# Optimization experiments

Measured on AMD Instinct MI355X. Metric: run time of the kernel, lower is better.

Reference implementation:

```python
import jax, jax.numpy as jnp
import numpy as np

B, S, HID, H, D, KC = 2, 4096, 2048, 16, 128, 4
EPS = 1e-5


def causal_dw_conv(x, kern):
    # x: (b, s, C); kern: (K, 1, C) depthwise causal conv
    K = kern.shape[0]
    xp = jnp.pad(x, ((0, 0), (K - 1, 0), (0, 0)))
    return jax.lax.conv_general_dilated(
        xp, kern, (1,), 'VALID',
        dimension_numbers=('NWC', 'WIO', 'NWC'),
        feature_group_count=x.shape[-1])


def l2norm(x):
    return x * jax.lax.rsqrt(jnp.sum(x * x, -1, keepdims=True) + 1e-6)


def chunk_delta(q, k, v, g, beta, chunk_size):
    # q,k,v,g: (b,s,h,d); beta: (b,s,h). Chunked gated delta-rule (WY repr).
    dt0 = q.dtype
    q = jnp.transpose(q, (0, 2, 1, 3)).astype(jnp.float32)
    k = jnp.transpose(k, (0, 2, 1, 3)).astype(jnp.float32)
    v = jnp.transpose(v, (0, 2, 1, 3)).astype(jnp.float32)
    g = jnp.transpose(g, (0, 2, 1, 3)).astype(jnp.float32)
    beta = jnp.transpose(beta, (0, 2, 1)).astype(jnp.float32)
    b, h, s, dk = k.shape
    dv = v.shape[-1]
    C = chunk_size
    pad = (C - s % C) % C
    if pad:
        p4 = ((0, 0), (0, 0), (0, pad), (0, 0))
        q = jnp.pad(q, p4); k = jnp.pad(k, p4)
        v = jnp.pad(v, p4); g = jnp.pad(g, p4)
        beta = jnp.pad(beta, ((0, 0), (0, 0), (0, pad)))
    n = (s + pad) // C
    q = q * dk ** -0.5

    def toc(x):  # (b,h,s,d) -> (n,b,h,C,d)
        return jnp.transpose(x.reshape(b, h, n, C, -1), (2, 0, 1, 3, 4))

    g_cum = jnp.cumsum(g.reshape(b, h, n, C, dk), axis=-2)  # per-chunk cumsum
    xs = (toc(q), toc(k), toc(v),
          jnp.transpose(g_cum, (2, 0, 1, 3, 4)),
          jnp.transpose(beta.reshape(b, h, n, C), (2, 0, 1, 3)))
    eye = jnp.eye(C, dtype=jnp.float32)
    strict = jnp.tril(jnp.ones((C, C), bool), -1)[:, :, None]  # i > j
    incl = jnp.tril(jnp.ones((C, C), bool))[:, :, None]        # i >= j
    neg_inf = -jnp.inf

    def body(Sst, xc):
        qc, kc, vc, g_i, bc = xc  # (b,h,C,dk/dv), bc (b,h,C)
        gd = g_i[..., :, None, :] - g_i[..., None, :, :]       # (b,h,C,C,dk)
        A = jnp.einsum('bhijd,bhid,bhjd->bhij',
                       jnp.exp(jnp.where(strict, gd, neg_inf)), kc, kc)
        A = A * bc[..., None]
        L = eye + A  # unit lower-triangular
        T = jax.scipy.linalg.solve_triangular(
            L, jnp.broadcast_to(eye, L.shape), lower=True)
        Tf = T * bc[..., None, :]
        u = Tf @ vc                           # (b,h,C,dv)
        w = Tf @ (kc * jnp.exp(g_i))          # (b,h,C,dk)
        v_new = u - w @ Sst                   # (b,h,C,dv)
        attn = jnp.einsum('bhijd,bhid,bhjd->bhij',
                          jnp.exp(jnp.where(incl, gd, neg_inf)), qc, kc)
        o = attn @ v_new + (qc * jnp.exp(g_i)) @ Sst
        g_last = g_i[..., -1:, :]             # (b,h,1,dk)
        k_tail = kc * jnp.exp(g_last - g_i)
        S_new = Sst * jnp.exp(g_last[..., 0, :])[..., None] \
              + jnp.einsum('bhcd,bhce->bhde', k_tail, v_new)
        return S_new, o

    S0 = jnp.zeros((b, h, dk, dv), jnp.float32)
    _, o = jax.lax.scan(jax.checkpoint(body), S0, xs)
    o = jnp.transpose(o, (1, 2, 0, 3, 4)).reshape(b, h, -1, dv)[:, :, :s]
    return jnp.transpose(o, (0, 2, 1, 3)).astype(dt0)


def _forward(hidden_states, Wq, Wk, Wv, conv_q, conv_k, conv_v, Wb,
             Wfa, Wfb, Wga, Wgb, bgb, A_log, dt_bias, rms_scale, Wo,
             chunk_size):
    x = hidden_states
    b, s, _ = x.shape
    q = jax.nn.silu(causal_dw_conv(x @ Wq, conv_q)).reshape(b, s, H, D)
    k = jax.nn.silu(causal_dw_conv(x @ Wk, conv_k)).reshape(b, s, H, D)
    v = jax.nn.silu(causal_dw_conv(x @ Wv, conv_v)).reshape(b, s, H, D)
    q, k = l2norm(q), l2norm(k)
    beta = jax.nn.sigmoid(x @ Wb)                     # (b,s,H)
    g_lin = (x @ Wfa) @ Wfb + dt_bias                 # fused KDA gate (log space)
    g = -jnp.exp(A_log) * jax.nn.softplus(
        g_lin.astype(jnp.float32)).reshape(b, s, H, D)
    core = chunk_delta(q, k, v, g, beta, chunk_size)  # (b,s,H,D)
    gate = ((x @ Wga) @ Wgb + bgb).reshape(b, s, H, D)
    cf = core.astype(jnp.float32)
    normed = cf * jax.lax.rsqrt(
        jnp.mean(cf * cf, -1, keepdims=True) + EPS) * rms_scale
    o = normed * jax.nn.sigmoid(gate.astype(jnp.float32))
    return o.reshape(b, s, H * D) @ Wo


def setup_inputs() -> dict:
    key = jax.random.key(0)
    ks = jax.random.split(key, 18)
    def w(k, shape, fan_in):
        return jax.random.normal(k, shape, jnp.float32) * fan_in ** -0.5
    return {
        'hidden_states': jax.random.normal(ks[0], (B, S, HID), jnp.float32),
        'Wq': w(ks[1], (HID, H * D), HID),
        'Wk': w(ks[2], (HID, H * D), HID),
        'Wv': w(ks[3], (HID, H * D), HID),
        'conv_q': w(ks[4], (KC, 1, H * D), KC),
        'conv_k': w(ks[5], (KC, 1, H * D), KC),
        'conv_v': w(ks[6], (KC, 1, H * D), KC),
        'Wb': w(ks[7], (HID, H), HID),
        'Wfa': w(ks[8], (HID, D), HID),
        'Wfb': w(ks[9], (D, H * D), D),
        'Wga': w(ks[10], (HID, D), HID),
        'Wgb': w(ks[11], (D, H * D), D),
        'bgb': jnp.zeros((H * D,), jnp.float32),
        'A_log': jnp.log(jax.random.uniform(ks[12], (1, 1, H, 1),
                                            jnp.float32, 0.5, 8.0)),
        'dt_bias': jnp.ones((H * D,), jnp.float32),
        'rms_scale': jnp.ones((D,), jnp.float32),
        'Wo': w(ks[13], (H * D, HID), H * D),
        'chunk_size': 64,
    }


def reference(hidden_states, Wq, Wk, Wv, conv_q, conv_k, conv_v, Wb,
              Wfa, Wfb, Wga, Wgb, bgb, A_log, dt_bias, rms_scale, Wo,
              chunk_size):
    return _forward(hidden_states, Wq, Wk, Wv, conv_q, conv_k, conv_v, Wb,
                    Wfa, Wfb, Wga, Wgb, bgb, A_log, dt_bias, rms_scale, Wo,
                    int(chunk_size))
```

## Files before the change

kernel.cpp:

```cpp
#include <hip/hip_runtime.h>
#include <hip/hip_bf16.h>

typedef __hip_bfloat16 bf16;
typedef __attribute__((ext_vector_type(4))) float f32x4;
typedef __attribute__((ext_vector_type(8))) short short8;

#define TOT   8192
#define SEQ   4096
#define NHD   16
#define HD    128
#define C2    2048
#define CHK   64
#define NCPB  64
#define SW    16
#define QSCALE 0.08838834764831845f

__device__ __forceinline__ float b2f(bf16 x){ return __bfloat162float(x); }
__device__ __forceinline__ bf16  f2b(float x){ return __float2bfloat16(x); }
__device__ __forceinline__ float expn(float x){ return __expf(fminf(x, 0.f)); }
__device__ __forceinline__ short bts(float x){
  bf16 b = f2b(x); short s; __builtin_memcpy(&s, &b, 2); return s;
}
__device__ __forceinline__ float s2f(short v){
  unsigned int u = ((unsigned int)(unsigned short)v) << 16;
  float f; __builtin_memcpy(&f, &u, 4); return f;
}

__device__ __attribute__((aligned(16))) unsigned short G_xb  [TOT*C2];
__device__ __attribute__((aligned(16))) unsigned short G_xlo [TOT*C2];
__device__ __attribute__((aligned(16))) unsigned short G_qlin[TOT*C2];
__device__ __attribute__((aligned(16))) unsigned short G_klin[TOT*C2];
__device__ __attribute__((aligned(16))) unsigned short G_vlin[TOT*C2];
__device__ __attribute__((aligned(16))) unsigned short G_qb  [TOT*C2];
__device__ __attribute__((aligned(16))) unsigned short G_kb  [TOT*C2];
__device__ __attribute__((aligned(16))) unsigned short G_vb  [TOT*C2];
__device__ __attribute__((aligned(16))) unsigned short G_qg  [TOT*C2];
__device__ __attribute__((aligned(16))) unsigned short G_gate[TOT*C2];
__device__ __attribute__((aligned(16))) unsigned short G_core[TOT*C2];
__device__ __attribute__((aligned(16))) unsigned short G_opre[TOT*C2];
__device__ __attribute__((aligned(16))) float          G_g   [TOT*C2];
__device__ __attribute__((aligned(16))) unsigned short G_attn[2048*CHK*CHK];
__device__ __attribute__((aligned(16))) unsigned short G_ktt [2048*CHK*HD];
__device__ __attribute__((aligned(16))) float          G_egl [2048*HD];
__device__ __attribute__((aligned(16))) float          G_beta[TOT*NHD];
__device__ __attribute__((aligned(16))) unsigned short G_fah [TOT*HD];
__device__ __attribute__((aligned(16))) unsigned short G_fal [TOT*HD];
__device__ __attribute__((aligned(16))) unsigned short G_ga  [TOT*HD];
__device__ __attribute__((aligned(16))) unsigned short G_Wqt [C2*C2];
__device__ __attribute__((aligned(16))) unsigned short G_Wkt [C2*C2];
__device__ __attribute__((aligned(16))) unsigned short G_Wvt [C2*C2];
__device__ __attribute__((aligned(16))) unsigned short G_Wot [C2*C2];
__device__ __attribute__((aligned(16))) unsigned short G_Wgat  [HD*C2];
__device__ __attribute__((aligned(16))) unsigned short G_Wbt   [16*C2];
__device__ __attribute__((aligned(16))) unsigned short G_Wfat_h[HD*C2];
__device__ __attribute__((aligned(16))) unsigned short G_Wfat_l[HD*C2];
__device__ __attribute__((aligned(16))) unsigned short G_Wfbt_h[C2*HD];
__device__ __attribute__((aligned(16))) unsigned short G_Wfbt_l[C2*HD];
__device__ __attribute__((aligned(16))) unsigned short G_Wgbt  [C2*HD];

#define P_QLIN ((bf16*)G_qlin)
#define P_KLIN ((bf16*)G_klin)
#define P_VLIN ((bf16*)G_vlin)
#define P_QB   ((bf16*)G_qb)
#define P_KB   ((bf16*)G_kb)
#define P_VB   ((bf16*)G_vb)
#define P_QG   ((bf16*)G_qg)
#define P_GATE ((bf16*)G_gate)
#define P_CORE ((bf16*)G_core)
#define P_OPRE ((bf16*)G_opre)
#define P_ATTN ((bf16*)G_attn)
#define P_KTT  ((bf16*)G_ktt)
#define P_FAH  ((bf16*)G_fah)
#define P_FAL  ((bf16*)G_fal)
#define P_GA   ((bf16*)G_ga)

__device__ __forceinline__ const bf16* selWt(int s){
  switch(s){ case 0: return (const bf16*)G_Wqt; case 1: return (const bf16*)G_Wkt;
             case 2: return (const bf16*)G_Wvt; }
  return (const bf16*)G_Wot;
}
__device__ __forceinline__ bf16* selCm(int s){
  switch(s){ case 0: return P_QLIN; case 1: return P_KLIN; }
  return P_VLIN;
}
__device__ __forceinline__ bf16* selWT(int s){
  switch(s){
    case 0: return (bf16*)G_Wqt;     case 1: return (bf16*)G_Wkt;
    case 2: return (bf16*)G_Wvt;     case 3: return (bf16*)G_Wot;
    case 4: return (bf16*)G_Wgat;    case 5: return (bf16*)G_Wbt;
    case 6: return (bf16*)G_Wfat_h;  case 7: return (bf16*)G_Wfat_l;
    case 8: return (bf16*)G_Wfbt_h;  case 9: return (bf16*)G_Wfbt_l;
  }
  return (bf16*)G_Wgbt;
}

__global__ void __launch_bounds__(256) wtrans_k(const float* __restrict__ W,
                                                int selH, int selL, int N, int K)
{
  __shared__ float tile[64][65];
  const int t = threadIdx.x;
  const int n0 = blockIdx.x*64, k0 = blockIdx.y*64;
  const int c4 = (t&15)*4, rr = t>>4;
  if (n0 + c4 < N){
    #pragma unroll
    for (int i=0;i<4;i++){
      const float* src = W + (size_t)(k0+rr+16*i)*N + n0 + c4;
      float4 f = *(const float4*)src;
      tile[rr+16*i][c4+0]=f.x; tile[rr+16*i][c4+1]=f.y;
      tile[rr+16*i][c4+2]=f.z; tile[rr+16*i][c4+3]=f.w;
    }
  }
  __syncthreads();
  bf16* outH = selWT(selH);
  bf16* outL = (selL >= 0) ? selWT(selL) : nullptr;
  const int nr = t>>3, kc = (t&7)*8;
  #pragma unroll
  for (int p=0;p<2;p++){
    int n = p*32 + nr;
    if (n0 + n < N){
      __attribute__((aligned(16))) bf16 tmpH[8];
      __attribute__((aligned(16))) bf16 tmpL[8];
      #pragma unroll
      for (int j=0;j<8;j++){
        float v = tile[kc+j][n];
        bf16 hh = f2b(v);
        tmpH[j] = hh;
        tmpL[j] = f2b(v - b2f(hh));
      }
      *(float4*)(outH + (size_t)(n0+n)*K + k0 + kc) = *(const float4*)tmpH;
      if (outL)
        *(float4*)(outL + (size_t)(n0+n)*K + k0 + kc) = *(const float4*)tmpL;
    }
  }
}

__global__ void __launch_bounds__(256) xconv_k(const float* __restrict__ x)
{
  size_t idx = ((size_t)blockIdx.x*256 + threadIdx.x)*8;
  const float* src = x + idx;
  float4 f0 = *(const float4*)src, f1 = *(const float4*)(src+4);
  float v[8] = {f0.x,f0.y,f0.z,f0.w,f1.x,f1.y,f1.z,f1.w};
  __attribute__((aligned(16))) bf16 th[8];
  __attribute__((aligned(16))) bf16 tl[8];
  #pragma unroll
  for (int u=0;u<8;u++){
    bf16 h = f2b(v[u]);
    th[u] = h;
    tl[u] = f2b(v[u] - b2f(h));
  }
  *(float4*)((bf16*)G_xb  + idx) = *(const float4*)th;
  *(float4*)((bf16*)G_xlo + idx) = *(const float4*)tl;
}

template<int OUTMODE>
__global__ void __launch_bounds__(256) gemm_mfma(
    int aSel, int bSel, int cSel, float* __restrict__ Cw, int N)
{
  const bf16* A  = (aSel==0) ? (const bf16*)G_xb : (const bf16*)G_opre;
  const bf16* Bt = selWt(bSel);
  __shared__ bf16 As[128*40];
  __shared__ bf16 Bs[128*40];
  const int t  = threadIdx.x;
  const int l  = t & 63;
  const int wv = t >> 6;
  const int wm = (wv>>1)*64, wn = (wv&1)*64;
  const int bm = blockIdx.y*128, bn = blockIdx.x*128;
  const int lr = l & 15;
  const int lk = (l>>4)*8;
  const int sr = t>>1, sc = (t&1)*16;

  f32x4 acc[4][4];
  #pragma unroll
  for (int i=0;i<4;i++)
    #pragma unroll
    for (int j=0;j<4;j++)
      #pragma unroll
      for (int v=0;v<4;v++) acc[i][j][v] = 0.f;

  for (int k0=0; k0<C2; k0+=32){
    const bf16* ga = A  + (size_t)(bm+sr)*C2 + k0 + sc;
    const bf16* gb = Bt + (size_t)(bn+sr)*C2 + k0 + sc;
    float4 a0 = *(const float4*)ga; float4 a1 = *(const float4*)(ga+8);
    float4 b0 = *(const float4*)gb; float4 b1 = *(const float4*)(gb+8);
    __syncthreads();
    *(float4*)&As[sr*40+sc]   = a0; *(float4*)&As[sr*40+sc+8] = a1;
    *(float4*)&Bs[sr*40+sc]   = b0; *(float4*)&Bs[sr*40+sc+8] = b1;
    __syncthreads();
    short8 af[4], bfr[4];
    #pragma unroll
    for (int i=0;i<4;i++){
      af[i]  = *(const short8*)&As[(wm+i*16+lr)*40 + lk];
      bfr[i] = *(const short8*)&Bs[(wn+i*16+lr)*40 + lk];
    }
    #pragma unroll
    for (int i=0;i<4;i++)
      #pragma unroll
      for (int j=0;j<4;j++)
        acc[i][j] = __builtin_amdgcn_mfma_f32_16x16x32_bf16(af[i], bfr[j], acc[i][j], 0, 0, 0);
  }

  bf16* Cb = (OUTMODE==0) ? selCm(cSel) : nullptr;
  #pragma unroll
  for (int i=0;i<4;i++){
    #pragma unroll
    for (int v=0;v<4;v++){
      int r = bm + wm + i*16 + (l>>4)*4 + v;
      #pragma unroll
      for (int j=0;j<4;j++){
        int col = bn + wn + j*16 + (l&15);
        float val = acc[i][j][v];
        if (OUTMODE==1) Cw[(size_t)r*N + col] = val;
        else            Cb[(size_t)r*N + col] = f2b(val);
      }
    }
  }
}

__global__ void __launch_bounds__(256) thinx_k()
{
  const int t = threadIdx.x;
  const int l = t & 63;
  const int wv = t >> 6;
  const int rb = wv >> 1, nh = wv & 1;
  const int lane16 = l & 15, quad = l >> 4;
  const int bm = blockIdx.x*32;
  const int arow = bm + rb*16 + lane16;

  const bf16* Ah = (const bf16*)G_xb  + (size_t)arow*C2;
  const bf16* Al = (const bf16*)G_xlo + (size_t)arow*C2;
  const bf16* Wfh = (const bf16*)G_Wfat_h;
  const bf16* Wfl = (const bf16*)G_Wfat_l;
  const bf16* Wg  = (const bf16*)G_Wgat;
  const bf16* Wbp = (const bf16*)G_Wbt;

  f32x4 accF[4], accG[4], accB;
  #pragma unroll
  for (int cb=0;cb<4;cb++)
    #pragma unroll
    for (int v=0;v<4;v++){ accF[cb][v]=0.f; accG[cb][v]=0.f; }
  #pragma unroll
  for (int v=0;v<4;v++) accB[v]=0.f;

  for (int k0=0; k0<C2; k0+=32){
    const int ko = k0 + quad*8;
    short8 ah = *(const short8*)(Ah + ko);
    short8 al = *(const short8*)(Al + ko);
    #pragma unroll
    for (int cb=0;cb<4;cb++){
      const size_t nrow = (size_t)(nh*64 + cb*16 + lane16)*C2 + ko;
      short8 bh = *(const short8*)(Wfh + nrow);
      short8 bl = *(const short8*)(Wfl + nrow);
      accF[cb] = __builtin_amdgcn_mfma_f32_16x16x32_bf16(ah, bh, accF[cb], 0,0,0);
      accF[cb] = __builtin_amdgcn_mfma_f32_16x16x32_bf16(ah, bl, accF[cb], 0,0,0);
      accF[cb] = __builtin_amdgcn_mfma_f32_16x16x32_bf16(al, bh, accF[cb], 0,0,0);
      short8 bg = *(const short8*)(Wg + nrow);
      accG[cb] = __builtin_amdgcn_mfma_f32_16x16x32_bf16(ah, bg, accG[cb], 0,0,0);
    }
    if (nh == 0){
      short8 bb = *(const short8*)(Wbp + (size_t)lane16*C2 + ko);
      accB = __builtin_amdgcn_mfma_f32_16x16x32_bf16(ah, bb, accB, 0,0,0);
    }
  }

  #pragma unroll
  for (int cb=0;cb<4;cb++){
    #pragma unroll
    for (int v=0;v<4;v++){
      int r = bm + rb*16 + quad*4 + v;
      int n = nh*64 + cb*16 + lane16;
      float vf = accF[cb][v];
      bf16 fh = f2b(vf);
      P_FAH[(size_t)r*HD + n] = fh;
      P_FAL[(size_t)r*HD + n] = f2b(vf - b2f(fh));
      P_GA [(size_t)r*HD + n] = f2b(accG[cb][v]);
    }
  }
  if (nh == 0){
    #pragma unroll
    for (int v=0;v<4;v++){
      int r = bm + rb*16 + quad*4 + v;
      G_beta[(size_t)r*NHD + lane16] = 1.f/(1.f + __expf(-accB[v]));
    }
  }
}

__global__ void __launch_bounds__(256) glin_k(const float* __restrict__ dtb)
{
  const int t = threadIdx.x;
  const int l = t & 63;
  const int wv = t >> 6;
  const int wm = (wv>>1)*64, wn = (wv&1)*64;
  const int bm = blockIdx.y*128, bn = blockIdx.x*128;
  const int lane16 = l & 15, quad = l >> 4;

  f32x4 acc[4][4];
  #pragma unroll
  for (int i=0;i<4;i++)
    #pragma unroll
    for (int j=0;j<4;j++)
      #pragma unroll
      for (int v=0;v<4;v++) acc[i][j][v]=0.f;

  #pragma unroll
  for (int pass=0; pass<3; ++pass){
    const bf16* A = (pass < 2) ? P_FAH : P_FAL;
    const bf16* B = (pass == 1) ? (const bf16*)G_Wfbt_l : (const bf16*)G_Wfbt_h;
    #pragma unroll
    for (int ks=0; ks<4; ++ks){
      short8 af[4], bfr[4];
      #pragma unroll
      for (int i=0;i<4;i++)
        af[i] = *(const short8*)(A + (size_t)(bm+wm+i*16+lane16)*HD + ks*32 + quad*8);
      #pragma unroll
      for (int j=0;j<4;j++)
        bfr[j] = *(const short8*)(B + (size_t)(bn+wn+j*16+lane16)*HD + ks*32 + quad*8);
      #pragma unroll
      for (int i=0;i<4;i++)
        #pragma unroll
        for (int j=0;j<4;j++)
          acc[i][j] = __builtin_amdgcn_mfma_f32_16x16x32_bf16(af[i], bfr[j], acc[i][j], 0,0,0);
    }
  }

  #pragma unroll
  for (int i=0;i<4;i++){
    #pragma unroll
    for (int v=0;v<4;v++){
      int r = bm + wm + i*16 + quad*4 + v;
      #pragma unroll
      for (int j=0;j<4;j++){
        int n = bn + wn + j*16 + lane16;
        G_g[(size_t)r*C2 + n] = acc[i][j][v] + dtb[n];
      }
    }
  }
}

__global__ void __launch_bounds__(256) gate_k(const float* __restrict__ bgb)
{
  const int t = threadIdx.x;
  const int l = t & 63;
  const int wv = t >> 6;
  const int wm = (wv>>1)*64, wn = (wv&1)*64;
  const int bm = blockIdx.y*128, bn = blockIdx.x*128;
  const int lane16 = l & 15, quad = l >> 4;

  f32x4 acc[4][4];
  #pragma unroll
  for (int i=0;i<4;i++)
    #pragma unroll
    for (int j=0;j<4;j++)
      #pragma unroll
      for (int v=0;v<4;v++) acc[i][j][v]=0.f;

  const bf16* A = P_GA;
  const bf16* B = (const bf16*)G_Wgbt;
  #pragma unroll
  for (int ks=0; ks<4; ++ks){
    short8 af[4], bfr[4];
    #pragma unroll
    for (int i=0;i<4;i++)
      af[i] = *(const short8*)(A + (size_t)(bm+wm+i*16+lane16)*HD + ks*32 + quad*8);
    #pragma unroll
    for (int j=0;j<4;j++)
      bfr[j] = *(const short8*)(B + (size_t)(bn+wn+j*16+lane16)*HD + ks*32 + quad*8);
    #pragma unroll
    for (int i=0;i<4;i++)
      #pragma unroll
      for (int j=0;j<4;j++)
        acc[i][j] = __builtin_amdgcn_mfma_f32_16x16x32_bf16(af[i], bfr[j], acc[i][j], 0,0,0);
  }

  #pragma unroll
  for (int i=0;i<4;i++){
    #pragma unroll
    for (int v=0;v<4;v++){
      int r = bm + wm + i*16 + quad*4 + v;
      #pragma unroll
      for (int j=0;j<4;j++){
        int n = bn + wn + j*16 + lane16;
        P_GATE[(size_t)r*C2 + n] = f2b(acc[i][j][v] + bgb[n]);
      }
    }
  }
}

__global__ void __launch_bounds__(256) conv_silu_k(
    int sel, const float* __restrict__ kern, int do_norm)
{
  const bf16* lin = sel==0 ? P_QLIN : sel==1 ? P_KLIN : P_VLIN;
  bf16*       out = sel==0 ? P_QB   : sel==1 ? P_KB   : P_VB;

  __shared__ float part[256];
  __shared__ float scal[16];
  const int t = threadIdx.x;
  const int r = blockIdx.x;
  const int s = r & (SEQ-1);
  const int c0 = t*8;
  float v[8];
  #pragma unroll
  for (int u=0;u<8;u++) v[u]=0.f;
  for (int j=0;j<4;j++){
    int sp = s - 3 + j;
    if (sp < 0) continue;
    const bf16* row = lin + (size_t)(r-3+j)*C2 + c0;
    const float* kr = kern + j*C2 + c0;
    #pragma unroll
    for (int u=0;u<8;u++) v[u] += b2f(row[u]) * kr[u];
  }
  #pragma unroll
  for (int u=0;u<8;u++){ float x=v[u]; v[u] = x / (1.f + __expf(-x)); }
  if (do_norm) {
    float ss=0.f;
    #pragma unroll
    for (int u=0;u<8;u++) ss += v[u]*v[u];
    part[t]=ss; __syncthreads();
    if (t<16){
      float s2=0.f;
      for (int i=0;i<16;i++) s2 += part[t*16+i];
      scal[t] = rsqrtf(s2 + 1e-6f);
    }
    __syncthreads();
    float sc = scal[t>>4];
    #pragma unroll
    for (int u=0;u<8;u++) v[u] *= sc;
  }
  bf16* orow = out + (size_t)r*C2 + c0;
  #pragma unroll
  for (int u=0;u<8;u++) orow[u] = f2b(v[u]);
}

__global__ void __launch_bounds__(256) g_transform_k(const float* __restrict__ A_log)
{
  size_t i = (size_t)blockIdx.x*256 + threadIdx.x;
  float x = fminf(G_g[i], 80.f);
  int h = (int)((i >> 7) & (NHD-1));
  float a = __expf(A_log[h]);
  float sp = (x > 20.f) ? x : log1pf(__expf(x));
  G_g[i] = -a * sp;
}

__global__ void __launch_bounds__(128) gcum_k()
{
  const int blk = blockIdx.x;
  const int icg = blk & 127, h = blk >> 7;
  const int d = threadIdx.x;
  size_t gi = (size_t)(icg*CHK)*C2 + h*HD + d;
  float a = 0.f;
  for (int r=0;r<CHK;r++){ a += G_g[gi]; G_g[gi] = a; gi += C2; }
}

__global__ void __launch_bounds__(512, 4) stage1_k()
{
  __shared__ __attribute__((aligned(16))) char sm[63872];
  bf16*  kT   = (bf16*)sm;
  bf16*  qT   = (bf16*)(sm+17408);
  float* AmD  = (float*)(sm+17408);
  float* AmL  = (float*)(sm+21760);
  float* gH   = (float*)(sm+34816);
  float* Dinv = (float*)(sm+34816);
  bf16*  cJ   = (bf16*)(sm+44544);
  float* rhs  = (float*)(sm+44544);
  float* rS   = (float*)(sm+57600);
  float* er   = (float*)(sm+61440);
  float* bcs  = (float*)(sm+63552);

  const int blk = blockIdx.x;
  const int h   = blk >> 7;
  const int icg = blk & 127;
  const int cid = blk;
  const int t   = threadIdx.x;
  const int l   = t & 63;
  const int wv  = t >> 6;
  const int lane16 = l & 15, quad = l >> 4;
  const size_t base = (size_t)(icg*CHK)*C2 + h*HD;

  const int ci_b = t >> 7;
  const int ck   = t & 127;
  int ci, cjj;
  {
    float fi = (sqrtf(8.f*(float)ck + 1.f) - 1.f)*0.5f;
    ci = (int)fi;
    cjj = ck - ((ci*(ci+1))>>1);
    if (cjj < 0){ ci--; cjj = ck - ((ci*(ci+1))>>1); }
    if (cjj > ci){ ci++; cjj = ck - ((ci*(ci+1))>>1); }
  }
  const int hasB = (ck < 8);
  const int bjB  = 8 + ck;

  #pragma unroll
  for (int it=0; it<2; ++it){
    int e = t + 512*it;
    int r = e >> 4, c8 = (e & 15)*8;
    *(float4*)&kT[r*136 + c8] = *(const float4*)(P_KB + base + (size_t)r*C2 + c8);
    *(float4*)&qT[r*136 + c8] = *(const float4*)(P_QB + base + (size_t)r*C2 + c8);
  }
  if (t < 64) bcs[t] = G_beta[(size_t)(icg*CHK + t)*NHD + h];

  float aaA=0.f, qqA=0.f, aaB=0.f, qqB=0.f;

  #pragma unroll 1
  for (int p=0; p<4; ++p){
    const int dq0 = p*32;
    __syncthreads();
    { int r = t >> 3, f4 = (t & 7)*4;
      float4 f = *(const float4*)(G_g + base + (size_t)r*C2 + dq0 + f4);
      gH[r*38 + f4+0] = f.x; gH[r*38 + f4+1] = f.y;
      gH[r*38 + f4+2] = f.z; gH[r*38 + f4+3] = f.w;
    }
    __syncthreads();
    if (t < 128){
      int I = t >> 5, dd = t & 31;
      float rv = gH[(I*16)*38 + dd];
      rS[I*132 + dq0 + dd] = rv;
      er[I*132 + dq0 + dd] = expn(rv);
    }
    if (t < 32) G_egl[(size_t)cid*HD + dq0 + t] = expn(gH[63*38 + t]);
    {
      const int rI = 16*ci_b + ci, rJ = 16*ci_b + cjj;
      const float* gRi = &gH[rI*38];
      const float* gRj = &gH[rJ*38];
      const bf16*  kRi = &kT[rI*136 + dq0];
      const bf16*  kRj = &kT[rJ*136 + dq0];
      const bf16*  qRi = &qT[rI*136 + dq0];
      float aa = aaA, qq = qqA;
      #pragma unroll 4
      for (int dd=0; dd<32; ++dd){
        float e  = expn(gRi[dd] - gRj[dd]);
        float tk = e * b2f(kRj[dd]);
        aa += tk * b2f(kRi[dd]);
        qq += tk * b2f(qRi[dd]);
      }
      aaA = aa; qqA = qq;
      if (hasB){
        const int rB = 16*ci_b + 15, rJ2 = 16*ci_b + bjB;
        const float* gRi2 = &gH[rB*38];
        const float* gRj2 = &gH[rJ2*38];
        const bf16*  kRi2 = &kT[rB*136 + dq0];
        const bf16*  kRj2 = &kT[rJ2*136 + dq0];
        const bf16*  qRi2 = &qT[rB*136 + dq0];
        float aa2 = aaB, qq2 = qqB;
        #pragma unroll 4
        for (int dd=0; dd<32; ++dd){
          float e  = expn(gRi2[dd] - gRj2[dd]);
          float tk = e * b2f(kRj2[dd]);
          aa2 += tk * b2f(kRi2[dd]);
          qq2 += tk * b2f(qRi2[dd]);
        }
        aaB = aa2; qqB = qq2;
      }
    }
    #pragma unroll
    for (int it=0; it<3; ++it){
      int e = t + 512*it;
      int r = e >> 5, dd = e & 31;
      float rv = gH[(((r>>4)+1)*16)*38 + dd];
      float v = b2f(kT[r*136 + dq0 + dd]) * expn(rv - gH[r*38 + dd]);
      cJ[r*136 + dq0 + dd] = f2b(v);
    }
    {
      int d = t >> 4, r4 = (t & 15)*4;
      float gl = gH[63*38 + d];
      __attribute__((aligned(8))) bf16 tmp[4];
      #pragma unroll
      for (int u=0; u<4; ++u){
        int r = r4 + u;
        tmp[u] = f2b(b2f(kT[r*136 + dq0 + d]) * expn(gl - gH[r*38 + d]));
      }
      *(float2*)(P_KTT + (size_t)cid*(CHK*HD) + (size_t)(dq0 + d)*64 + r4) =
          *(const float2*)tmp;
    }
    __syncthreads();
    #pragma unroll
    for (int it=0; it<4; ++it){
      int e = t + 512*it;
      int r = e >> 5, dd = e & 31;
      int I = r >> 4;
      float eD  = expn(gH[r*38 + dd] - gH[(I*16)*38 + dd]);
      float erv = er[I*132 + dq0 + dd];
      int idx = r*136 + dq0 + dd;
      float av = b2f(kT[idx]) * eD;
      kT[idx] = f2b(av);
      float qv = QSCALE * b2f(qT[idx]) * eD;
      qT[idx] = f2b(qv);
      P_QG[base + (size_t)r*C2 + dq0 + dd] = f2b(qv * erv);
    }
  }
  __syncthreads();

  short8 bfr[4];
  int pI = 0, pJ = 0;
  {
    const int PI_[6] = {1,2,2,3,3,3};
    const int PJ_[6] = {0,0,1,0,1,2};
    if (wv < 6){
      pI = PI_[wv]; pJ = PJ_[wv];
      #pragma unroll
      for (int ks=0; ks<4; ++ks){
        int k0 = ks*32 + quad*8;
        short8 raw = *(const short8*)&cJ[(16*pJ + lane16)*136 + k0];
        short8 o;
        #pragma unroll
        for (int u=0; u<8; ++u){
          int d = k0 + u;
          float m = expn(rS[pI*132 + d] - rS[(pJ+1)*132 + d]);
          o[u] = bts(s2f(raw[u]) * m);
        }
        bfr[ks] = o;
      }
      f32x4 acc;
      #pragma unroll
      for (int v=0; v<4; ++v) acc[v] = 0.f;
      #pragma unroll
      for (int ks=0; ks<4; ++ks){
        short8 af = *(const short8*)&qT[(16*pI + lane16)*136 + ks*32 + quad*8];
        acc = __builtin_amdgcn_mfma_f32_16x16x32_bf16(af, bfr[ks], acc, 0,0,0);
      }
      #pragma unroll
      for (int v=0; v<4; ++v){
        int row = 16*pI + quad*4 + v, col = 16*pJ + lane16;
        P_ATTN[(size_t)cid*4096 + row*64 + col] = f2b(acc[v]);
      }
    } else {
      const int UI_[6] = {0,0,0,1,1,2};
      const int UJ_[6] = {1,2,3,2,3,3};
      float4 zf; zf.x = zf.y = zf.z = zf.w = 0.f;
      int tt = t - 384;
      for (int e = tt; e < 192; e += 128){
        int b = e >> 5, row = (e>>1)&15, hf = e&1;
        *(float4*)(P_ATTN + (size_t)cid*4096 +
                   (size_t)((16*UI_[b]+row)*64 + 16*UJ_[b] + hf*8)) = zf;
      }
    }
    size_t ab = (size_t)cid*4096;
    int rA = 16*ci_b + ci, cA = 16*ci_b + cjj;
    P_ATTN[ab + rA*64 + cA] = f2b(qqA * QSCALE);
    if (ci != cjj) P_ATTN[ab + cA*64 + rA] = f2b(0.f);
    if (hasB){
      int rB = 16*ci_b + 15, cB = 16*ci_b + bjB;
      P_ATTN[ab + rB*64 + cB] = f2b(qqB * QSCALE);
      if (bjB != 15) P_ATTN[ab + cB*64 + rB] = f2b(0.f);
    }
  }
  __syncthreads();

  if (wv < 6){
    f32x4 acc;
    #pragma unroll
    for (int v=0; v<4; ++v) acc[v] = 0.f;
    #pragma unroll
    for (int ks=0; ks<4; ++ks){
      short8 af = *(const short8*)&kT[(16*pI + lane16)*136 + ks*32 + quad*8];
      acc = __builtin_amdgcn_mfma_f32_16x16x32_bf16(af, bfr[ks], acc, 0,0,0);
    }
    #pragma unroll
    for (int v=0; v<4; ++v){
      int r16 = quad*4 + v;
      AmL[wv*272 + r16*17 + lane16] = acc[v] * bcs[16*pI + r16];
    }
  }
  if (ci != cjj) AmD[ci_b*272 + ci*17 + cjj] = aaA * bcs[16*ci_b + ci];
  if (hasB && bjB != 15) AmD[ci_b*272 + 15*17 + bjB] = aaB * bcs[16*ci_b + 15];
  __syncthreads();

  if (wv == 0){
    const int b = l >> 4, col = l & 15;
    const float* Ab = &AmD[b*272];
    float x[16];
    #pragma unroll
    for (int i=0; i<16; ++i){
      float a = (i == col) ? 1.f : 0.f;
      #pragma unroll
      for (int kk=0; kk<i; ++kk)
        a -= Ab[i*17 + kk] * x[kk];
      x[i] = a;
      Dinv[b*272 + i*17 + col] = a;
    }
  }

  #pragma unroll 1
  for (int inst=0; inst<4; ++inst){
    const int isW = inst >> 1;
    const int c0  = (inst & 1) * 64;
    __syncthreads();
    {
      const int r = t >> 3, c8 = (t & 7)*8;
      const float bcv = bcs[r];
      if (!isW){
        float4 f = *(const float4*)(P_VB + base + (size_t)r*C2 + c0 + c8);
        const bf16* e8 = (const bf16*)&f;
        #pragma unroll
        for (int u=0; u<8; ++u) rhs[r*66 + c8 + u] = b2f(e8[u]) * bcv;
      } else {
        const int I = r >> 4;
        #pragma unroll
        for (int u=0; u<8; ++u){
          int d = c0 + c8 + u;
          rhs[r*66 + c8 + u] = b2f(kT[r*136 + d]) * er[I*132 + d] * bcv;
        }
      }
    }
    __syncthreads();
    #pragma unroll 1
    for (int I=0; I<4; ++I){
      if (I > 0){
        #pragma unroll
        for (int e2=0; e2<2; ++e2){
          int slot = t + 512*e2;
          int r16 = slot >> 6, c = slot & 63;
          float a = rhs[(16*I + r16)*66 + c];
          #pragma unroll 1
          for (int J=0; J<I; ++J){
            const float* Arow = &AmL[(J + ((I*(I-1))>>1))*272 + r16*17];
            #pragma unroll
            for (int kk=0; kk<16; ++kk)
              a -= Arow[kk] * rhs[(16*J + kk)*66 + c];
          }
          rhs[(16*I + r16)*66 + c] = a;
        }
        __syncthreads();
      }
      float accv[2];
      #pragma unroll
      for (int e2=0; e2<2; ++e2){
        int slot = t + 512*e2;
        int r16 = slot >> 6, c = slot & 63;
        const float* Drow = &Dinv[I*272 + r16*17];
        float a = 0.f;
        #pragma unroll
        for (int kk=0; kk<16; ++kk)
          a += Drow[kk] * rhs[(16*I + kk)*66 + c];
        accv[e2] = a;
      }
      __syncthreads();
      #pragma unroll
      for (int e2=0; e2<2; ++e2){
        int slot = t + 512*e2;
        rhs[(16*I + (slot>>6))*66 + (slot & 63)] = accv[e2];
      }
      __syncthreads();
    }
    {
      const int r = t >> 3, c8 = (t & 7)*8;
      __attribute__((aligned(16))) bf16 tmp[8];
      #pragma unroll
      for (int u=0; u<8; ++u) tmp[u] = f2b(rhs[r*66 + c8 + u]);
      bf16* dst = isW ? P_QB : P_VB;
      *(float4*)(dst + base + (size_t)r*C2 + c0 + c8) = *(const float4*)tmp;
    }
  }
}

__global__ void __launch_bounds__(256) stage2_k()
{
  __shared__ float Sf[SW][HD+4];
  __shared__ bf16  wqL[CHK][HD+8];
  __shared__ bf16  ktL[HD][CHK+8];
  __shared__ bf16  ashL[CHK][CHK+8];
  __shared__ bf16  vnT[SW][CHK+8];
  __shared__ bf16  uL[CHK][SW+4];
  __shared__ float egl[HD];

  const int blk = blockIdx.x;
  const int batch = blk >> 7;
  const int h  = (blk >> 3) & 15;
  const int sl = blk & 7;
  const int c0 = sl*SW;
  const int t  = threadIdx.x;
  const int l  = t & 63;
  const int wv = t >> 6;
  const int lane16 = l & 15, quad = l >> 4;
  const int R = wv*16;

  for (int i=t;i<SW*(HD+4);i+=256) ((float*)Sf)[i] = 0.f;

  for (int ic=0; ic<NCPB; ic++){
    const int icg = batch*NCPB + ic;
    const int cid = h*128 + icg;
    const size_t rbase = (size_t)(icg*CHK)*C2 + h*HD;

    float4 qgr[4];
    #pragma unroll
    for (int it=0; it<4; ++it){
      int e = (t + 256*it)*8;
      int r = e >> 7, d = e & 127;
      *(float4*)&wqL[r][d] = *(const float4*)(P_QB + rbase + (size_t)r*C2 + d);
      qgr[it] = *(const float4*)(P_QG + rbase + (size_t)r*C2 + d);
    }
    {
      const bf16* src = P_KTT + (size_t)cid*(CHK*HD);
      #pragma unroll
      for (int it=0; it<4; ++it){
        int e = (t + 256*it)*8;
        int d = e >> 6, r = e & 63;
        *(float4*)&ktL[d][r] = *(const float4*)(src + e);
      }
      const bf16* asrc = P_ATTN + (size_t)cid*(CHK*CHK);
      #pragma unroll
      for (int it=0; it<2; ++it){
        int e = (t + 256*it)*8;
        int i2 = e >> 6, j2 = e & 63;
        *(float4*)&ashL[i2][j2] = *(const float4*)(asrc + e);
      }
      int r = t>>2, c = (t&3)*4;
      const bf16* us = P_VB + rbase + (size_t)r*C2 + c0 + c;
      uL[r][c]=us[0]; uL[r][c+1]=us[1]; uL[r][c+2]=us[2]; uL[r][c+3]=us[3];
      if (t < HD) egl[t] = G_egl[(size_t)cid*HD + t];
    }
    __syncthreads();

    {
      f32x4 acc1;
      #pragma unroll
      for (int v=0;v<4;v++) acc1[v]=0.f;
      #pragma unroll
      for (int ks=0; ks<4; ++ks){
        const int k0 = ks*32;
        short8 af = *(const short8*)&wqL[R+lane16][k0 + quad*8];
        short8 bfr;
        #pragma unroll
        for (int j2=0;j2<8;j2++) bfr[j2] = bts(Sf[lane16][k0 + quad*8 + j2]);
        acc1 = __builtin_amdgcn_mfma_f32_16x16x32_bf16(af, bfr, acc1, 0,0,0);
      }
      #pragma unroll
      for (int v=0;v<4;v++){
        int j = R + quad*4 + v;
        float x = b2f(uL[j][lane16]) - acc1[v];
        vnT[lane16][j] = f2b(x);
      }
    }
    __syncthreads();

    #pragma unroll
    for (int it=0; it<4; ++it){
      int e = (t + 256*it)*8;
      int r = e >> 7, d = e & 127;
      *(float4*)&wqL[r][d] = qgr[it];
    }
    __syncthreads();

    {
      f32x4 acc2;
      #pragma unroll
      for (int v=0;v<4;v++) acc2[v]=0.f;
      #pragma unroll
      for (int ks=0; ks<2; ++ks){
        const int k0 = ks*32;
        short8 af = *(const short8*)&ashL[R+lane16][k0 + quad*8];
        short8 bfr = *(const short8*)&vnT[lane16][k0 + quad*8];
        acc2 = __builtin_amdgcn_mfma_f32_16x16x32_bf16(af, bfr, acc2, 0,0,0);
      }
      #pragma unroll
      for (int ks=0; ks<4; ++ks){
        const int k0 = ks*32;
        short8 af = *(const short8*)&wqL[R+lane16][k0 + quad*8];
        short8 bfr;
        #pragma unroll
        for (int j2=0;j2<8;j2++) bfr[j2] = bts(Sf[lane16][k0 + quad*8 + j2]);
        acc2 = __builtin_amdgcn_mfma_f32_16x16x32_bf16(af, bfr, acc2, 0,0,0);
      }
      #pragma unroll
      for (int v=0;v<4;v++){
        size_t row = (size_t)(icg*CHK) + R + quad*4 + v;
        P_CORE[row*C2 + h*HD + c0 + lane16] = f2b(acc2[v]);
      }
    }
    {
      f32x4 accS[2];
      #pragma unroll
      for (int p=0;p<2;p++)
        #pragma unroll
        for (int v=0;v<4;v++) accS[p][v]=0.f;
      #pragma unroll
      for (int p=0;p<2;p++){
        const int dt = wv*2 + p;
        #pragma unroll
        for (int ks=0; ks<2; ++ks){
          const int k0 = ks*32;
          short8 af = *(const short8*)&ktL[dt*16 + lane16][k0 + quad*8];
          short8 bfr = *(const short8*)&vnT[lane16][k0 + quad*8];
          accS[p] = __builtin_amdgcn_mfma_f32_16x16x32_bf16(af, bfr, accS[p], 0,0,0);
        }
      }
      __syncthreads();
      #pragma unroll
      for (int p=0;p<2;p++){
        #pragma unroll
        for (int v=0;v<4;v++){
          int d = (wv*2+p)*16 + quad*4 + v;
          Sf[lane16][d] = Sf[lane16][d]*egl[d] + accS[p][v];
        }
      }
    }
  }
}

__global__ void __launch_bounds__(256) rms_gate_k(const float* __restrict__ rms)
{
  __shared__ float part[256];
  __shared__ float scal[16];
  const int t = threadIdx.x;
  const size_t tok = blockIdx.x;
  const int c0 = t*8;
  float v[8];
  const bf16* cr = P_CORE + tok*C2 + c0;
  #pragma unroll
  for (int u=0;u<8;u++) v[u] = b2f(cr[u]);
  float ss=0.f;
  #pragma unroll
  for (int u=0;u<8;u++) ss += v[u]*v[u];
  part[t]=ss; __syncthreads();
  if (t<16){
    float s2=0.f;
    for (int i=0;i<16;i++) s2 += part[t*16+i];
    scal[t] = rsqrtf(s2*(1.f/HD) + 1e-5f);
  }
  __syncthreads();
  float sc = scal[t>>4];
  const bf16* gr = P_GATE + tok*C2 + c0;
  bf16* orow = P_OPRE + tok*C2 + c0;
  #pragma unroll
  for (int u=0;u<8;u++){
    int d = (c0+u)&127;
    float gv = b2f(gr[u]);
    float x = v[u]*sc*rms[d];
    x *= 1.f/(1.f+__expf(-gv));
    orow[u] = f2b(x);
  }
}

extern "C" void kernel_launch(void* const* d_in, const int* in_sizes, int n_in,
                              void* d_out, int out_size, void* d_ws, size_t ws_size,
                              hipStream_t stream)
{
  const float* x     = (const float*)d_in[0];
  const float* Wq    = (const float*)d_in[1];
  const float* Wk    = (const float*)d_in[2];
  const float* Wv    = (const float*)d_in[3];
  const float* convq = (const float*)d_in[4];
  const float* convk = (const float*)d_in[5];
  const float* convv = (const float*)d_in[6];
  const float* Wb    = (const float*)d_in[7];
  const float* Wfa   = (const float*)d_in[8];
  const float* Wfb   = (const float*)d_in[9];
  const float* Wga   = (const float*)d_in[10];
  const float* Wgb   = (const float*)d_in[11];
  const float* bgb   = (const float*)d_in[12];
  const float* A_log = (const float*)d_in[13];
  const float* dtb   = (const float*)d_in[14];
  const float* rms   = (const float*)d_in[15];
  const float* Wo    = (const float*)d_in[16];
  (void)d_ws; (void)ws_size;

  dim3 gM(16, TOT/128);
  dim3 gN(16, TOT/128);

  wtrans_k<<<dim3(32,32), 256, 0, stream>>>(Wq,  0, -1, C2,  C2);
  wtrans_k<<<dim3(32,32), 256, 0, stream>>>(Wk,  1, -1, C2,  C2);
  wtrans_k<<<dim3(32,32), 256, 0, stream>>>(Wv,  2, -1, C2,  C2);
  wtrans_k<<<dim3(32,32), 256, 0, stream>>>(Wo,  3, -1, C2,  C2);
  wtrans_k<<<dim3(2,32),  256, 0, stream>>>(Wga, 4, -1, HD,  C2);
  wtrans_k<<<dim3(1,32),  256, 0, stream>>>(Wb,  5, -1, NHD, C2);
  wtrans_k<<<dim3(2,32),  256, 0, stream>>>(Wfa, 6,  7, HD,  C2);
  wtrans_k<<<dim3(32,2),  256, 0, stream>>>(Wfb, 8,  9, C2,  HD);
  wtrans_k<<<dim3(32,2),  256, 0, stream>>>(Wgb, 10,-1, C2,  HD);

  xconv_k<<<TOT*C2/(256*8), 256, 0, stream>>>(x);

  gemm_mfma<0><<<gM, 256, 0, stream>>>(0, 0, 0, nullptr, C2);
  gemm_mfma<0><<<gM, 256, 0, stream>>>(0, 1, 1, nullptr, C2);
  gemm_mfma<0><<<gM, 256, 0, stream>>>(0, 2, 2, nullptr, C2);

  thinx_k<<<TOT/32, 256, 0, stream>>>();

  conv_silu_k<<<TOT, 256, 0, stream>>>(0, convq, 1);
  conv_silu_k<<<TOT, 256, 0, stream>>>(1, convk, 1);
  conv_silu_k<<<TOT, 256, 0, stream>>>(2, convv, 0);

  glin_k<<<gN, 256, 0, stream>>>(dtb);
  g_transform_k<<<(TOT*C2)/256, 256, 0, stream>>>(A_log);
  gcum_k<<<2048, 128, 0, stream>>>();

  stage1_k<<<2048, 512, 0, stream>>>();
  stage2_k<<<256, 256, 0, stream>>>();

  gate_k<<<gN, 256, 0, stream>>>(bgb);
  rms_gate_k<<<TOT, 256, 0, stream>>>(rms);

  gemm_mfma<1><<<gM, 256, 0, stream>>>(1, 3, -1, (float*)d_out, C2);
}
```

Measured before the change: 1.575 ms.

## Use direct-to-LDS loads in GEMM, fuse g transform, restructure stage1 diagonal

The main GEMM now loads A and B tiles with global_load_lds straight into unpadded LDS and swizzles block order into groups of eight for cache locality. The separate g_transform kernel is folded into the glin_k epilogue, which saves a full fp32 read and write pass over the g tensor. In stage1, the diagonal-block intra-chunk dot products are remapped so each thread handles a pair of adjacent columns with vectorized loads. Removing the LDS padding may add bank conflicts on the fragment reads, and the GEMM still uses a single LDS buffer with no double buffering.

```diff
diff --git a/kernel.cpp b/kernel.cpp
--- a/kernel.cpp
+++ b/kernel.cpp
@@ -24,6 +24,12 @@
 __device__ __forceinline__ float s2f(short v){
   unsigned int u = ((unsigned int)(unsigned short)v) << 16;
   float f; __builtin_memcpy(&f, &u, 4); return f;
+}
+__device__ __forceinline__ void gload_lds16(const void* g, void* l){
+  __builtin_amdgcn_global_load_lds(
+    (const __attribute__((address_space(1))) unsigned int*)g,
+    (__attribute__((address_space(3))) unsigned int*)l,
+    16, 0, 0);
 }
 
 __device__ __attribute__((aligned(16))) unsigned short G_xb  [TOT*C2];
@@ -158,16 +164,23 @@
 {
   const bf16* A  = (aSel==0) ? (const bf16*)G_xb : (const bf16*)G_opre;
   const bf16* Bt = selWt(bSel);
-  __shared__ bf16 As[128*40];
-  __shared__ bf16 Bs[128*40];
+  __shared__ bf16 As[128*32];
+  __shared__ bf16 Bs[128*32];
   const int t  = threadIdx.x;
   const int l  = t & 63;
   const int wv = t >> 6;
   const int wm = (wv>>1)*64, wn = (wv&1)*64;
-  const int bm = blockIdx.y*128, bn = blockIdx.x*128;
+
+  const int nbx = gridDim.x;
+  const int tot = nbx * gridDim.y;
+  const int id  = blockIdx.y*nbx + blockIdx.x;
+  const int cpx = tot >> 3;
+  const int sw  = (id & 7)*cpx + (id >> 3);
+  const int bm  = (sw / nbx)*128, bn = (sw % nbx)*128;
+
   const int lr = l & 15;
   const int lk = (l>>4)*8;
-  const int sr = t>>1, sc = (t&1)*16;
+  const int srow = l >> 2, scol = (l & 3)*8;
 
   f32x4 acc[4][4];
   #pragma unroll
@@ -178,19 +191,19 @@
       for (int v=0;v<4;v++) acc[i][j][v] = 0.f;
 
   for (int k0=0; k0<C2; k0+=32){
-    const bf16* ga = A  + (size_t)(bm+sr)*C2 + k0 + sc;
-    const bf16* gb = Bt + (size_t)(bn+sr)*C2 + k0 + sc;
-    float4 a0 = *(const float4*)ga; float4 a1 = *(const float4*)(ga+8);
-    float4 b0 = *(const float4*)gb; float4 b1 = *(const float4*)(gb+8);
     __syncthreads();
-    *(float4*)&As[sr*40+sc]   = a0; *(float4*)&As[sr*40+sc+8] = a1;
-    *(float4*)&Bs[sr*40+sc]   = b0; *(float4*)&Bs[sr*40+sc+8] = b1;
+    #pragma unroll
+    for (int i=0;i<2;i++){
+      const int rb = wv*32 + i*16;
+      gload_lds16(A  + (size_t)(bm + rb + srow)*C2 + k0 + scol, &As[rb*32]);
+      gload_lds16(Bt + (size_t)(bn + rb + srow)*C2 + k0 + scol, &Bs[rb*32]);
+    }
     __syncthreads();
     short8 af[4], bfr[4];
     #pragma unroll
     for (int i=0;i<4;i++){
-      af[i]  = *(const short8*)&As[(wm+i*16+lr)*40 + lk];
-      bfr[i] = *(const short8*)&Bs[(wn+i*16+lr)*40 + lk];
+      af[i]  = *(const short8*)&As[(wm+i*16+lr)*32 + lk];
+      bfr[i] = *(const short8*)&Bs[(wn+i*16+lr)*32 + lk];
     }
     #pragma unroll
     for (int i=0;i<4;i++)
@@ -284,7 +297,8 @@
   }
 }
 
-__global__ void __launch_bounds__(256) glin_k(const float* __restrict__ dtb)
+__global__ void __launch_bounds__(256) glin_k(const float* __restrict__ dtb,
+                                              const float* __restrict__ A_log)
 {
   const int t = threadIdx.x;
   const int l = t & 63;
@@ -323,14 +337,18 @@
   }
 
   #pragma unroll
-  for (int i=0;i<4;i++){
-    #pragma unroll
-    for (int v=0;v<4;v++){
-      int r = bm + wm + i*16 + quad*4 + v;
-      #pragma unroll
-      for (int j=0;j<4;j++){
-        int n = bn + wn + j*16 + lane16;
-        G_g[(size_t)r*C2 + n] = acc[i][j][v] + dtb[n];
+  for (int j=0;j<4;j++){
+    const int n = bn + wn + j*16 + lane16;
+    const float dtv = dtb[n];
+    const float av = __expf(A_log[(n>>7)&(NHD-1)]);
+    #pragma unroll
+    for (int i=0;i<4;i++){
+      #pragma unroll
+      for (int v=0;v<4;v++){
+        int r = bm + wm + i*16 + quad*4 + v;
+        float x = fminf(acc[i][j][v] + dtv, 80.f);
+        float sp = (x > 20.f) ? x : log1pf(__expf(x));
+        G_g[(size_t)r*C2 + n] = -av * sp;
       }
     }
   }
@@ -428,16 +446,6 @@
   bf16* orow = out + (size_t)r*C2 + c0;
   #pragma unroll
   for (int u=0;u<8;u++) orow[u] = f2b(v[u]);
-}
-
-__global__ void __launch_bounds__(256) g_transform_k(const float* __restrict__ A_log)
-{
-  size_t i = (size_t)blockIdx.x*256 + threadIdx.x;
-  float x = fminf(G_g[i], 80.f);
-  int h = (int)((i >> 7) & (NHD-1));
-  float a = __expf(A_log[h]);
-  float sp = (x > 20.f) ? x : log1pf(__expf(x));
-  G_g[i] = -a * sp;
 }
 
 __global__ void __launch_bounds__(128) gcum_k()
@@ -475,18 +483,20 @@
   const int lane16 = l & 15, quad = l >> 4;
   const size_t base = (size_t)(icg*CHK)*C2 + h*HD;
 
-  const int ci_b = t >> 7;
-  const int ck   = t & 127;
-  int ci, cjj;
-  {
-    float fi = (sqrtf(8.f*(float)ck + 1.f) - 1.f)*0.5f;
-    ci = (int)fi;
-    cjj = ck - ((ci*(ci+1))>>1);
-    if (cjj < 0){ ci--; cjj = ck - ((ci*(ci+1))>>1); }
-    if (cjj > ci){ ci++; cjj = ck - ((ci*(ci+1))>>1); }
-  }
-  const int hasB = (ck < 8);
-  const int bjB  = 8 + ck;
+  const bool dvalid = (t < 288);
+  int dbq = 0, di = 0, dj0 = 0;
+  bool dhas1 = false;
+  if (dvalid){
+    dbq = t / 72;
+    int s = t - dbq*72;
+    #pragma unroll
+    for (int m=0;m<16;m++){
+      int np = (m+2)>>1;
+      if (s >= np){ s -= np; di = m+1; }
+    }
+    dj0 = 2*s;
+    dhas1 = (dj0 + 1 <= di);
+  }
 
   #pragma unroll
   for (int it=0; it<2; ++it){
@@ -497,7 +507,7 @@
   }
   if (t < 64) bcs[t] = G_beta[(size_t)(icg*CHK + t)*NHD + h];
 
-  float aaA=0.f, qqA=0.f, aaB=0.f, qqB=0.f;
+  float aa0=0.f, qq0=0.f, aa1=0.f, qq1=0.f;
 
   #pragma unroll 1
   for (int p=0; p<4; ++p){
@@ -516,38 +526,34 @@
       er[I*132 + dq0 + dd] = expn(rv);
     }
     if (t < 32) G_egl[(size_t)cid*HD + dq0 + t] = expn(gH[63*38 + t]);
-    {
-      const int rI = 16*ci_b + ci, rJ = 16*ci_b + cjj;
-      const float* gRi = &gH[rI*38];
-      const float* gRj = &gH[rJ*38];
-      const bf16*  kRi = &kT[rI*136 + dq0];
-      const bf16*  kRj = &kT[rJ*136 + dq0];
-      const bf16*  qRi = &qT[rI*136 + dq0];
-      float aa = aaA, qq = qqA;
-      #pragma unroll 4
-      for (int dd=0; dd<32; ++dd){
-        float e  = expn(gRi[dd] - gRj[dd]);
-        float tk = e * b2f(kRj[dd]);
-        aa += tk * b2f(kRi[dd]);
-        qq += tk * b2f(qRi[dd]);
-      }
-      aaA = aa; qqA = qq;
-      if (hasB){
-        const int rB = 16*ci_b + 15, rJ2 = 16*ci_b + bjB;
-        const float* gRi2 = &gH[rB*38];
-        const float* gRj2 = &gH[rJ2*38];
-        const bf16*  kRi2 = &kT[rB*136 + dq0];
-        const bf16*  kRj2 = &kT[rJ2*136 + dq0];
-        const bf16*  qRi2 = &qT[rB*136 + dq0];
-        float aa2 = aaB, qq2 = qqB;
-        #pragma unroll 4
-        for (int dd=0; dd<32; ++dd){
-          float e  = expn(gRi2[dd] - gRj2[dd]);
-          float tk = e * b2f(kRj2[dd]);
-          aa2 += tk * b2f(kRi2[dd]);
-          qq2 += tk * b2f(qRi2[dd]);
+
+    if (dvalid){
+      const int rI = 16*dbq + di, rJ = 16*dbq + dj0;
+      const int rJ1 = (rJ + 1 < 64) ? rJ + 1 : 63;
+      const float* gRi  = &gH[rI*38];
+      const float* gRj  = &gH[rJ*38];
+      const float* gRj1 = &gH[rJ1*38];
+      #pragma unroll
+      for (int c8=0; c8<32; c8+=8){
+        float gi[8], gj[8], gj1[8];
+        #pragma unroll
+        for (int u2=0; u2<4; ++u2){
+          float2 a0 = *(const float2*)&gRi[c8+u2*2];  gi[u2*2]=a0.x;  gi[u2*2+1]=a0.y;
+          float2 a1 = *(const float2*)&gRj[c8+u2*2];  gj[u2*2]=a1.x;  gj[u2*2+1]=a1.y;
+          float2 a2 = *(const float2*)&gRj1[c8+u2*2]; gj1[u2*2]=a2.x; gj1[u2*2+1]=a2.y;
         }
-        aaB = aa2; qqB = qq2;
+        short8 ki  = *(const short8*)&kT[rI*136 + dq0 + c8];
+        short8 qi  = *(const short8*)&qT[rI*136 + dq0 + c8];
+        short8 kj  = *(const short8*)&kT[rJ*136 + dq0 + c8];
+        short8 kj1 = *(const short8*)&kT[rJ1*136 + dq0 + c8];
+        #pragma unroll
+        for (int u=0; u<8; ++u){
+          float kiv = s2f(ki[u]), qiv = s2f(qi[u]);
+          float e0 = expn(gi[u]-gj[u]) * s2f(kj[u]);
+          aa0 += e0*kiv; qq0 += e0*qiv;
+          float e1 = expn(gi[u]-gj1[u]) * s2f(kj1[u]);
+          aa1 += e1*kiv; qq1 += e1*qiv;
+        }
       }
     }
     #pragma unroll
@@ -632,14 +638,15 @@
                    (size_t)((16*UI_[b]+row)*64 + 16*UJ_[b] + hf*8)) = zf;
       }
     }
-    size_t ab = (size_t)cid*4096;
-    int rA = 16*ci_b + ci, cA = 16*ci_b + cjj;
-    P_ATTN[ab + rA*64 + cA] = f2b(qqA * QSCALE);
-    if (ci != cjj) P_ATTN[ab + cA*64 + rA] = f2b(0.f);
-    if (hasB){
-      int rB = 16*ci_b + 15, cB = 16*ci_b + bjB;
-      P_ATTN[ab + rB*64 + cB] = f2b(qqB * QSCALE);
-      if (bjB != 15) P_ATTN[ab + cB*64 + rB] = f2b(0.f);
+    if (dvalid){
+      size_t ab = (size_t)cid*4096;
+      int rA = 16*dbq + di, cA = 16*dbq + dj0;
+      P_ATTN[ab + rA*64 + cA] = f2b(qq0 * QSCALE);
+      if (dj0 < di) P_ATTN[ab + cA*64 + rA] = f2b(0.f);
+      if (dhas1){
+        P_ATTN[ab + rA*64 + cA+1] = f2b(qq1 * QSCALE);
+        if (dj0+1 < di) P_ATTN[ab + (cA+1)*64 + rA] = f2b(0.f);
+      }
     }
   }
   __syncthreads();
@@ -659,8 +666,11 @@
       AmL[wv*272 + r16*17 + lane16] = acc[v] * bcs[16*pI + r16];
     }
   }
-  if (ci != cjj) AmD[ci_b*272 + ci*17 + cjj] = aaA * bcs[16*ci_b + ci];
-  if (hasB && bjB != 15) AmD[ci_b*272 + 15*17 + bjB] = aaB * bcs[16*ci_b + 15];
+  if (dvalid){
+    float bcv = bcs[16*dbq + di];
+    if (dj0 < di) AmD[dbq*272 + di*17 + dj0] = aa0 * bcv;
+    if (dhas1 && dj0+1 < di) AmD[dbq*272 + di*17 + dj0+1] = aa1 * bcv;
+  }
   __syncthreads();
 
   if (wv == 0){
@@ -977,8 +987,7 @@
   conv_silu_k<<<TOT, 256, 0, stream>>>(1, convk, 1);
   conv_silu_k<<<TOT, 256, 0, stream>>>(2, convv, 0);
 
-  glin_k<<<gN, 256, 0, stream>>>(dtb);
-  g_transform_k<<<(TOT*C2)/256, 256, 0, stream>>>(A_log);
+  glin_k<<<gN, 256, 0, stream>>>(dtb, A_log);
   gcum_k<<<2048, 128, 0, stream>>>();
 
   stage1_k<<<2048, 512, 0, stream>>>();
```

New measurement: 1.860 ms. 18.0% more time.
